# Kernel optimization log

Hardware: AMD Instinct MI355X
Metric: run time of the kernel (lower is better)

The kernel has to match this reference:

```python
import jax, jax.numpy as jnp
import numpy as np
import math

EPS = 1e-6
MAX_NORM = 1.0 - 1e-3


def _clip_to_ball(x):
    # Keep point strictly inside the unit ball (||x|| < 1).
    norm = jnp.maximum(jnp.linalg.norm(x, axis=-1, keepdims=True), EPS)
    factor = jnp.minimum(MAX_NORM / norm, 1.0)
    return x * factor


def setup_inputs() -> dict:
    key = jax.random.key(0)
    k1, k2 = jax.random.split(key)
    B, C, D = 8192, 4096, 512
    euclidean_emb = jax.random.normal(k1, (B, D), dtype=jnp.float32)
    centroids = jax.random.uniform(k2, (C, D), dtype=jnp.float32, minval=-0.01, maxval=0.01)
    log_c = jnp.asarray(math.log(1.0), dtype=jnp.float32)
    return {"euclidean_emb": euclidean_emb, "log_c": log_c, "centroids": centroids}


def reference(euclidean_emb, log_c, centroids):
    # torch code used c = self.log_c.exp().item() -> c is detached scalar
    c = jax.lax.stop_gradient(jnp.exp(log_c))
    sqrt_c = jnp.sqrt(c)

    # expmap0: Euclidean -> Poincare ball
    v_norm = jnp.maximum(jnp.linalg.norm(euclidean_emb, axis=-1, keepdims=True), EPS)
    coeff = jnp.tanh(sqrt_c * v_norm) / (sqrt_c * v_norm)
    x_h = _clip_to_ball(coeff * euclidean_emb)   # (B, D)
    cen_h = _clip_to_ball(centroids)             # (C, D)

    # Pairwise Poincare distance via GEMM (same math as the expanded (B,C,D) form):
    # ||x - y||^2 = ||x||^2 + ||y||^2 - 2 <x, y>
    x2_raw = jnp.sum(x_h * x_h, axis=-1)         # (B,)
    y2_raw = jnp.sum(cen_h * cen_h, axis=-1)     # (C,)
    x2 = jnp.minimum(x2_raw, MAX_NORM ** 2)
    y2 = jnp.minimum(y2_raw, MAX_NORM ** 2)
    xy = x_h @ cen_h.T                           # (B, C) GEMM
    diff2 = x2_raw[:, None] + y2_raw[None, :] - 2.0 * xy

    denom = jnp.maximum((1.0 - c * x2)[:, None] * (1.0 - c * y2)[None, :], EPS)
    arg = jnp.maximum(1.0 + c * (2.0 * diff2) / denom, 1.0 + EPS)
    dists = jnp.arccosh(arg) / sqrt_c            # (B, C)
    return dists, x_h, cen_h
```

## Files before the change

### kernel.cpp

```cpp
#include <hip/hip_runtime.h>
#include <math.h>

#define EPSV 1e-6f
#define MAX_NORM (1.0f - 1e-3f)

typedef __attribute__((ext_vector_type(8))) short short8;
typedef __attribute__((ext_vector_type(4))) float f32x4;

__device__ inline ushort f32_to_bf16(float f) {
    union { float f; uint32_t u; } cv;
    cv.f = f;
    uint32_t u = cv.u;
    u += 0x7FFFu + ((u >> 16) & 1u);
    return (ushort)(u >> 16);
}

__device__ inline void glds16(const ushort* gsrc, ushort* ldsdst) {
    auto* g = (const __attribute__((address_space(1))) uint32_t*)gsrc;
    auto* l = (__attribute__((address_space(3))) uint32_t*)ldsdst;
    __builtin_amdgcn_global_load_lds(g, l, 16, 0, 0);
}

__device__ inline short8 ds_read128(const ushort* p) {
    auto* l3 = (const __attribute__((address_space(3))) ushort*)p;
    const uint32_t addr = (uint32_t)(uintptr_t)l3;
    short8 v;
    asm volatile("ds_read_b128 %0, %1" : "=&v"(v) : "v"(addr));
    return v;
}

__device__ inline size_t pack_off(int r, int j) {
    return ((size_t)(r >> 4) * 16 + (j >> 2)) * 512
         + (size_t)(((j & 3) * 16 + (r & 15)) * 8);
}

__global__ void rows_emb_kernel(const float* __restrict__ emb,
                                const float* __restrict__ logc,
                                float* __restrict__ xh,
                                ushort* __restrict__ xpk,
                                float* __restrict__ x2raw,
                                float* __restrict__ dxv) {
    const int D = 512;
    const int row = blockIdx.x;
    const int lane = threadIdx.x;

    const float4* r4 = (const float4*)(emb + (size_t)row * D);
    float4 a = r4[2 * lane];
    float4 b = r4[2 * lane + 1];

    float ss = a.x * a.x + a.y * a.y + a.z * a.z + a.w * a.w
             + b.x * b.x + b.y * b.y + b.z * b.z + b.w * b.w;
#pragma unroll
    for (int off = 32; off > 0; off >>= 1) ss += __shfl_xor(ss, off, 64);

    const float c  = expf(logc[0]);
    const float sc = sqrtf(c);

    const float tn    = sqrtf(ss);
    const float vn    = fmaxf(tn, EPSV);
    const float coeff = tanhf(sc * vn) / (sc * vn);
    const float pre   = coeff * tn;
    const float fac   = fminf(MAX_NORM / fmaxf(pre, EPSV), 1.0f);
    const float scale = coeff * fac;

    float4 oa, ob;
    oa.x = a.x * scale; oa.y = a.y * scale; oa.z = a.z * scale; oa.w = a.w * scale;
    ob.x = b.x * scale; ob.y = b.y * scale; ob.z = b.z * scale; ob.w = b.w * scale;

    float4* o4 = (float4*)(xh + (size_t)row * D);
    o4[2 * lane]     = oa;
    o4[2 * lane + 1] = ob;

    union { ushort u[8]; uint4 v; } pk;
    pk.u[0] = f32_to_bf16(oa.x); pk.u[1] = f32_to_bf16(oa.y);
    pk.u[2] = f32_to_bf16(oa.z); pk.u[3] = f32_to_bf16(oa.w);
    pk.u[4] = f32_to_bf16(ob.x); pk.u[5] = f32_to_bf16(ob.y);
    pk.u[6] = f32_to_bf16(ob.z); pk.u[7] = f32_to_bf16(ob.w);
    *(uint4*)(xpk + pack_off(row, lane)) = pk.v;

    if (lane == 0) {
        const float sq = scale * scale * ss;
        x2raw[row] = sq;
        dxv[row]   = 1.0f - c * fminf(sq, MAX_NORM * MAX_NORM);
    }
}

__global__ void rows_cen_kernel(const float* __restrict__ cen,
                                const float* __restrict__ logc,
                                float* __restrict__ ch,
                                ushort* __restrict__ cpk,
                                float* __restrict__ y2raw,
                                float* __restrict__ dyv) {
    const int D = 512;
    const int row = blockIdx.x;
    const int lane = threadIdx.x;

    const float4* r4 = (const float4*)(cen + (size_t)row * D);
    float4 a = r4[2 * lane];
    float4 b = r4[2 * lane + 1];

    float ss = a.x * a.x + a.y * a.y + a.z * a.z + a.w * a.w
             + b.x * b.x + b.y * b.y + b.z * b.z + b.w * b.w;
#pragma unroll
    for (int off = 32; off > 0; off >>= 1) ss += __shfl_xor(ss, off, 64);

    const float c = expf(logc[0]);

    const float tn    = sqrtf(ss);
    const float scale = fminf(MAX_NORM / fmaxf(tn, EPSV), 1.0f);

    float4 oa, ob;
    oa.x = a.x * scale; oa.y = a.y * scale; oa.z = a.z * scale; oa.w = a.w * scale;
    ob.x = b.x * scale; ob.y = b.y * scale; ob.z = b.z * scale; ob.w = b.w * scale;

    float4* o4 = (float4*)(ch + (size_t)row * D);
    o4[2 * lane]     = oa;
    o4[2 * lane + 1] = ob;

    union { ushort u[8]; uint4 v; } pk;
    pk.u[0] = f32_to_bf16(oa.x); pk.u[1] = f32_to_bf16(oa.y);
    pk.u[2] = f32_to_bf16(oa.z); pk.u[3] = f32_to_bf16(oa.w);
    pk.u[4] = f32_to_bf16(ob.x); pk.u[5] = f32_to_bf16(ob.y);
    pk.u[6] = f32_to_bf16(ob.z); pk.u[7] = f32_to_bf16(ob.w);
    *(uint4*)(cpk + pack_off(row, lane)) = pk.v;

    if (lane == 0) {
        const float sq = scale * scale * ss;
        y2raw[row] = sq;
        dyv[row]   = 1.0f - c * fminf(sq, MAX_NORM * MAX_NORM);
    }
}

#define BM 256
#define BN 256
#define BKT 32
#define EPST 68
#define KDIM 512
#define NT 16
#define NCOLS 4096

__global__ __launch_bounds__(512, 1)
void gemm_epi_kernel(const ushort* __restrict__ Apk,
                     const ushort* __restrict__ Bpk,
                     const float* __restrict__ x2raw,
                     const float* __restrict__ dxv,
                     const float* __restrict__ y2raw,
                     const float* __restrict__ dyv,
                     const float* __restrict__ logc,
                     float* __restrict__ out) {
    __shared__ __align__(16) ushort ring[3 * 16384];

    const int tid  = threadIdx.x;
    const int lane = tid & 63;
    const int wid  = tid >> 6;
    const int wm   = wid >> 2;
    const int wn   = wid & 3;

    const int bm = blockIdx.y;
    const int bn = blockIdx.x;

    f32x4 acc[8][4];
#pragma unroll
    for (int m = 0; m < 8; m++)
#pragma unroll
        for (int n = 0; n < 4; n++) acc[m][n] = (f32x4){0.f, 0.f, 0.f, 0.f};

    const ushort* gA0 = Apk + ((size_t)(bm * 16 + 2 * wid)) * 8192 + lane * 8;
    const ushort* gA1 = gA0 + 8192;
    const ushort* gB0 = Bpk + ((size_t)(bn * 16 + 2 * wid)) * 8192 + lane * 8;
    const ushort* gB1 = gB0 + 8192;

    ushort* lA = &ring[0]    + wid * 1024;
    ushort* lB = &ring[8192] + wid * 1024;

    const ushort* rdA = &ring[0]    + wm * 4096 + lane * 8;
    const ushort* rdB = &ring[8192] + wn * 2048 + lane * 8;

    auto stage_tile = [&](int r, int t) {
        const int ko = t * 512;
        glds16(gA0 + ko, lA + r * 16384);
        glds16(gA1 + ko, lA + r * 16384 + 512);
        glds16(gB0 + ko, lB + r * 16384);
        glds16(gB1 + ko, lB + r * 16384 + 512);
    };

    stage_tile(0, 0);
    stage_tile(1, 1);

    for (int t = 0; t < NT; ++t) {
        if (t < NT - 1) asm volatile("s_waitcnt vmcnt(4)" ::: "memory");
        else            asm volatile("s_waitcnt vmcnt(0)" ::: "memory");
        __builtin_amdgcn_s_barrier();

        const int r16 = (t % 3) * 16384;
        const ushort* rA = rdA + r16;
        const ushort* rB = rdB + r16;

        const bool st  = (t + 2 < NT);
        const int  sr  = ((t + 2) % 3) * 16384;
        const int  sko = (t + 2) * 512;

        short8 bf[4];

#pragma unroll
        for (int q = 0; q < 4; ++q) {
            short8 a0, a1;
            if (q == 0) {
#pragma unroll
                for (int n = 0; n < 4; n++)
                    bf[n] = ds_read128(rB + n * 512);
            }
            a0 = ds_read128(rA + (2 * q) * 512);
            a1 = ds_read128(rA + (2 * q + 1) * 512);

            if (st) {
                if (q == 0) glds16(gA0 + sko, lA + sr);
                if (q == 1) glds16(gA1 + sko, lA + sr + 512);
                if (q == 2) glds16(gB0 + sko, lB + sr);
                if (q == 3) glds16(gB1 + sko, lB + sr + 512);
            }

            __builtin_amdgcn_s_barrier();
            asm volatile("s_waitcnt lgkmcnt(0)" ::: "memory");
            __builtin_amdgcn_sched_barrier(0);
            __builtin_amdgcn_s_setprio(1);
#pragma unroll
            for (int n = 0; n < 4; n++) {
                acc[2 * q][n]     = __builtin_amdgcn_mfma_f32_16x16x32_bf16(
                    a0, bf[n], acc[2 * q][n], 0, 0, 0);
                acc[2 * q + 1][n] = __builtin_amdgcn_mfma_f32_16x16x32_bf16(
                    a1, bf[n], acc[2 * q + 1][n], 0, 0, 0);
            }
            __builtin_amdgcn_sched_barrier(0);
            __builtin_amdgcn_s_setprio(0);
            __builtin_amdgcn_s_barrier();
        }
    }

    __syncthreads();

    const float c   = expf(logc[0]);
    const float rsc = 1.0f / sqrtf(c);
    const int l16 = lane & 15;
    const int lg  = lane >> 4;

    float* ep = (float*)((char*)&ring[0] + (size_t)wid * 4352);
    const int gr_base = bm * BM + wm * 128;
    const int gc_base = bn * BN + wn * 64;

#pragma unroll
    for (int m = 0; m < 8; m++) {
#pragma unroll
        for (int n = 0; n < 4; n++)
#pragma unroll
            for (int r = 0; r < 4; r++)
                ep[(lg * 4 + r) * EPST + n * 16 + l16] = acc[m][n][r];
        asm volatile("s_waitcnt lgkmcnt(0)" ::: "memory");

#pragma unroll
        for (int it = 0; it < 4; it++) {
            const int row = it * 4 + lg;
            const int gr  = gr_base + m * 16 + row;
            const int gc  = gc_base + l16 * 4;
            float4 xy4 = *(const float4*)&ep[row * EPST + l16 * 4];
            const float rx  = x2raw[gr];
            const float dxr = dxv[gr];
            const float4 ry4 = *(const float4*)&y2raw[gc];
            const float4 dy4 = *(const float4*)&dyv[gc];
            float4 o;
            {
                const float rden = __builtin_amdgcn_rcpf(fmaxf(dxr * dy4.x, EPSV));
                float t = fmaxf(2.0f * c * (rx + ry4.x - 2.0f * xy4.x) * rden, EPSV);
                o.x = __logf(1.0f + t + __builtin_amdgcn_sqrtf(t * (t + 2.0f))) * rsc;
            }
            {
                const float rden = __builtin_amdgcn_rcpf(fmaxf(dxr * dy4.y, EPSV));
                float t = fmaxf(2.0f * c * (rx + ry4.y - 2.0f * xy4.y) * rden, EPSV);
                o.y = __logf(1.0f + t + __builtin_amdgcn_sqrtf(t * (t + 2.0f))) * rsc;
            }
            {
                const float rden = __builtin_amdgcn_rcpf(fmaxf(dxr * dy4.z, EPSV));
                float t = fmaxf(2.0f * c * (rx + ry4.z - 2.0f * xy4.z) * rden, EPSV);
                o.z = __logf(1.0f + t + __builtin_amdgcn_sqrtf(t * (t + 2.0f))) * rsc;
            }
            {
                const float rden = __builtin_amdgcn_rcpf(fmaxf(dxr * dy4.w, EPSV));
                float t = fmaxf(2.0f * c * (rx + ry4.w - 2.0f * xy4.w) * rden, EPSV);
                o.w = __logf(1.0f + t + __builtin_amdgcn_sqrtf(t * (t + 2.0f))) * rsc;
            }
            *(float4*)&out[(size_t)gr * NCOLS + gc] = o;
        }
        asm volatile("s_waitcnt lgkmcnt(0)" ::: "memory");
    }
}

extern "C" void kernel_launch(void* const* d_in, const int* in_sizes, int n_in,
                              void* d_out, int out_size, void* d_ws, size_t ws_size,
                              hipStream_t stream) {
    const float* emb  = (const float*)d_in[0];
    const float* logc = (const float*)d_in[1];
    const float* cen  = (const float*)d_in[2];

    const int D = 512;
    const int B = in_sizes[0] / D;
    const int C = in_sizes[2] / D;

    float* out   = (float*)d_out;
    float* dists = out;
    float* xh    = out + (size_t)B * C;
    float* ch    = xh + (size_t)B * D;

    char* ws = (char*)d_ws;
    size_t off = 0;
    auto alloc = [&](size_t bytes) -> char* {
        char* p = ws + off;
        off += (bytes + 255) & ~(size_t)255;
        return p;
    };
    ushort* xpk   = (ushort*)alloc((size_t)B * D * sizeof(ushort));
    ushort* cpk   = (ushort*)alloc((size_t)C * D * sizeof(ushort));
    float*  x2raw = (float*)alloc((size_t)B * sizeof(float));
    float*  dxv   = (float*)alloc((size_t)B * sizeof(float));
    float*  y2raw = (float*)alloc((size_t)C * sizeof(float));
    float*  dyv   = (float*)alloc((size_t)C * sizeof(float));

    rows_emb_kernel<<<B, 64, 0, stream>>>(emb, logc, xh, xpk, x2raw, dxv);
    rows_cen_kernel<<<C, 64, 0, stream>>>(cen, logc, ch, cpk, y2raw, dyv);

    dim3 grid(C / BN, B / BM);
    gemm_epi_kernel<<<grid, 512, 0, stream>>>(xpk, cpk, x2raw, dxv, y2raw, dyv,
                                              logc, dists);
}
```

Before: 87.04 us.

## Load B fragments straight into registers and double-buffer A in LDS

B tiles no longer go through LDS. Each wave loads its own B fragments from global memory into registers, double-buffered across k-tiles. A is staged in a two-slot LDS double buffer instead of the three-slot ring, with one barrier per tile instead of several per quarter. The goal is to cut LDS traffic and barrier overhead. In exchange, B is loaded redundantly across the waves that share a column group, more VGPRs are used, and waiting on vmcnt(0) each tile reduces how much the prefetch overlaps with compute.

```diff
diff --git a/kernel.cpp b/kernel.cpp
--- a/kernel.cpp
+++ b/kernel.cpp
@@ -26,6 +26,12 @@
     const uint32_t addr = (uint32_t)(uintptr_t)l3;
     short8 v;
     asm volatile("ds_read_b128 %0, %1" : "=&v"(v) : "v"(addr));
+    return v;
+}
+
+__device__ inline short8 gload16(const ushort* p) {
+    short8 v;
+    asm volatile("global_load_dwordx4 %0, %1, off" : "=&v"(v) : "v"(p));
     return v;
 }
 
@@ -133,7 +139,6 @@
 
 #define BM 256
 #define BN 256
-#define BKT 32
 #define EPST 68
 #define KDIM 512
 #define NT 16
@@ -148,7 +153,8 @@
                      const float* __restrict__ dyv,
                      const float* __restrict__ logc,
                      float* __restrict__ out) {
-    __shared__ __align__(16) ushort ring[3 * 16384];
+    __shared__ __align__(16) char smem[36864];
+    ushort* Asm = (ushort*)smem;
 
     const int tid  = threadIdx.x;
     const int lane = tid & 63;
@@ -167,75 +173,83 @@
 
     const ushort* gA0 = Apk + ((size_t)(bm * 16 + 2 * wid)) * 8192 + lane * 8;
     const ushort* gA1 = gA0 + 8192;
-    const ushort* gB0 = Bpk + ((size_t)(bn * 16 + 2 * wid)) * 8192 + lane * 8;
-    const ushort* gB1 = gB0 + 8192;
-
-    ushort* lA = &ring[0]    + wid * 1024;
-    ushort* lB = &ring[8192] + wid * 1024;
-
-    const ushort* rdA = &ring[0]    + wm * 4096 + lane * 8;
-    const ushort* rdB = &ring[8192] + wn * 2048 + lane * 8;
-
-    auto stage_tile = [&](int r, int t) {
-        const int ko = t * 512;
-        glds16(gA0 + ko, lA + r * 16384);
-        glds16(gA1 + ko, lA + r * 16384 + 512);
-        glds16(gB0 + ko, lB + r * 16384);
-        glds16(gB1 + ko, lB + r * 16384 + 512);
-    };
-
-    stage_tile(0, 0);
-    stage_tile(1, 1);
-
-    for (int t = 0; t < NT; ++t) {
-        if (t < NT - 1) asm volatile("s_waitcnt vmcnt(4)" ::: "memory");
-        else            asm volatile("s_waitcnt vmcnt(0)" ::: "memory");
-        __builtin_amdgcn_s_barrier();
-
-        const int r16 = (t % 3) * 16384;
-        const ushort* rA = rdA + r16;
-        const ushort* rB = rdB + r16;
-
-        const bool st  = (t + 2 < NT);
-        const int  sr  = ((t + 2) % 3) * 16384;
-        const int  sko = (t + 2) * 512;
-
-        short8 bf[4];
-
-#pragma unroll
-        for (int q = 0; q < 4; ++q) {
-            short8 a0, a1;
-            if (q == 0) {
-#pragma unroll
-                for (int n = 0; n < 4; n++)
-                    bf[n] = ds_read128(rB + n * 512);
-            }
-            a0 = ds_read128(rA + (2 * q) * 512);
-            a1 = ds_read128(rA + (2 * q + 1) * 512);
-
-            if (st) {
-                if (q == 0) glds16(gA0 + sko, lA + sr);
-                if (q == 1) glds16(gA1 + sko, lA + sr + 512);
-                if (q == 2) glds16(gB0 + sko, lB + sr);
-                if (q == 3) glds16(gB1 + sko, lB + sr + 512);
-            }
-
-            __builtin_amdgcn_s_barrier();
-            asm volatile("s_waitcnt lgkmcnt(0)" ::: "memory");
-            __builtin_amdgcn_sched_barrier(0);
-            __builtin_amdgcn_s_setprio(1);
-#pragma unroll
-            for (int n = 0; n < 4; n++) {
-                acc[2 * q][n]     = __builtin_amdgcn_mfma_f32_16x16x32_bf16(
-                    a0, bf[n], acc[2 * q][n], 0, 0, 0);
-                acc[2 * q + 1][n] = __builtin_amdgcn_mfma_f32_16x16x32_bf16(
-                    a1, bf[n], acc[2 * q + 1][n], 0, 0, 0);
-            }
-            __builtin_amdgcn_sched_barrier(0);
-            __builtin_amdgcn_s_setprio(0);
-            __builtin_amdgcn_s_barrier();
-        }
+    ushort* lA = Asm + wid * 1024;
+
+    const ushort* gB = Bpk + ((size_t)(bn * 16 + wn * 4)) * 8192 + lane * 8;
+
+    const ushort* rdA = Asm + wm * 4096 + lane * 8;
+
+    short8 bX[4], bY[4];
+
+    glds16(gA0, lA);
+    glds16(gA1, lA + 512);
+#pragma unroll
+    for (int n = 0; n < 4; n++) bX[n] = gload16(gB + n * 8192);
+
+#define TILE_BODY(T, PAR, BCUR, BNXT)                                         \
+    do {                                                                      \
+        asm volatile("s_waitcnt vmcnt(0)" ::: "memory");                      \
+        __builtin_amdgcn_sched_barrier(0);                                    \
+        __builtin_amdgcn_s_barrier();                                         \
+        if ((T) + 1 < NT) {                                                   \
+            const int ko = ((T) + 1) * 512;                                   \
+            BNXT[0] = gload16(gB + 0 * 8192 + ko);                            \
+            BNXT[1] = gload16(gB + 1 * 8192 + ko);                            \
+            BNXT[2] = gload16(gB + 2 * 8192 + ko);                            \
+            BNXT[3] = gload16(gB + 3 * 8192 + ko);                            \
+            glds16(gA0 + ko, lA + (((T) + 1) & 1) * 8192);                    \
+            glds16(gA1 + ko, lA + (((T) + 1) & 1) * 8192 + 512);              \
+        }                                                                     \
+        const ushort* rA = rdA + (PAR) * 8192;                                \
+        short8 a0 = ds_read128(rA);                                           \
+        short8 a1 = ds_read128(rA + 512);                                     \
+        short8 a2 = ds_read128(rA + 1024);                                    \
+        short8 a3 = ds_read128(rA + 1536);                                    \
+        short8 a4 = ds_read128(rA + 2048);                                    \
+        short8 a5 = ds_read128(rA + 2560);                                    \
+        short8 a6 = ds_read128(rA + 3072);                                    \
+        short8 a7 = ds_read128(rA + 3584);                                    \
+        asm volatile("s_waitcnt lgkmcnt(4)" ::: "memory");                    \
+        __builtin_amdgcn_sched_barrier(0);                                    \
+        __builtin_amdgcn_s_setprio(1);                                        \
+        _Pragma("unroll")                                                     \
+        for (int n = 0; n < 4; n++) {                                         \
+            acc[0][n] = __builtin_amdgcn_mfma_f32_16x16x32_bf16(              \
+                a0, BCUR[n], acc[0][n], 0, 0, 0);                             \
+            acc[1][n] = __builtin_amdgcn_mfma_f32_16x16x32_bf16(              \
+                a1, BCUR[n], acc[1][n], 0, 0, 0);                             \
+            acc[2][n] = __builtin_amdgcn_mfma_f32_16x16x32_bf16(              \
+                a2, BCUR[n], acc[2][n], 0, 0, 0);                             \
+            acc[3][n] = __builtin_amdgcn_mfma_f32_16x16x32_bf16(              \
+                a3, BCUR[n], acc[3][n], 0, 0, 0);                             \
+        }                                                                     \
+        __builtin_amdgcn_sched_barrier(0);                                    \
+        __builtin_amdgcn_s_setprio(0);                                        \
+        asm volatile("s_waitcnt lgkmcnt(0)" ::: "memory");                    \
+        __builtin_amdgcn_sched_barrier(0);                                    \
+        __builtin_amdgcn_s_setprio(1);                                        \
+        _Pragma("unroll")                                                     \
+        for (int n = 0; n < 4; n++) {                                         \
+            acc[4][n] = __builtin_amdgcn_mfma_f32_16x16x32_bf16(              \
+                a4, BCUR[n], acc[4][n], 0, 0, 0);                             \
+            acc[5][n] = __builtin_amdgcn_mfma_f32_16x16x32_bf16(              \
+                a5, BCUR[n], acc[5][n], 0, 0, 0);                             \
+            acc[6][n] = __builtin_amdgcn_mfma_f32_16x16x32_bf16(              \
+                a6, BCUR[n], acc[6][n], 0, 0, 0);                             \
+            acc[7][n] = __builtin_amdgcn_mfma_f32_16x16x32_bf16(              \
+                a7, BCUR[n], acc[7][n], 0, 0, 0);                             \
+        }                                                                     \
+        __builtin_amdgcn_sched_barrier(0);                                    \
+        __builtin_amdgcn_s_setprio(0);                                        \
+    } while (0)
+
+#pragma unroll 1
+    for (int i = 0; i < NT / 2; ++i) {
+        const int te = 2 * i;
+        TILE_BODY(te,     0, bX, bY);
+        TILE_BODY(te + 1, 1, bY, bX);
     }
+#undef TILE_BODY
 
     __syncthreads();
 
@@ -244,7 +258,7 @@
     const int l16 = lane & 15;
     const int lg  = lane >> 4;
 
-    float* ep = (float*)((char*)&ring[0] + (size_t)wid * 4352);
+    float* ep = (float*)(smem + (size_t)wid * 4352);
     const int gr_base = bm * BM + wm * 128;
     const int gc_base = bn * BN + wn * 64;
 
```

New measurement: 83.85 us. 1.04x faster.
